# Kernel optimization log

Measured on AMD Instinct MI355X. Metric: run time of the kernel, lower is better.

The kernel has to match this reference:

```python
import jax, jax.numpy as jnp
import numpy as np

N, E, D, L = 100000, 600000, 128, 4
BN_EPS = 1e-5


def setup_inputs() -> dict:
    key = jax.random.key(0)
    ks = jax.random.split(key, 16)
    s = 0.02
    inp = {
        "x": jax.random.normal(ks[0], (N, D), dtype=jnp.float32),
        "edge_index": jax.random.randint(ks[1], (2, E), 0, N, dtype=jnp.int64),
        # per-layer SAGEConv params (lin_l has bias, lin_r has no bias in PyG)
        "lin_l_w": jax.random.normal(ks[2], (L, D, D), dtype=jnp.float32) * s,
        "lin_l_b": jnp.zeros((L, D), dtype=jnp.float32),
        "lin_r_w": jax.random.normal(ks[3], (L, D, D), dtype=jnp.float32) * s,
        # BatchNorm affine params (eval mode, running mean=0 var=1)
        "bn_w": jnp.ones((L, D), dtype=jnp.float32),
        "bn_b": jnp.zeros((L, D), dtype=jnp.float32),
        # MLP head: 128 -> 256 -> 128 -> 1
        "fc1_w": jax.random.normal(ks[4], (2 * D, D), dtype=jnp.float32) * s,
        "fc1_b": jnp.zeros((2 * D,), dtype=jnp.float32),
        "fc2_w": jax.random.normal(ks[5], (D, 2 * D), dtype=jnp.float32) * s,
        "fc2_b": jnp.zeros((D,), dtype=jnp.float32),
        "fc3_w": jax.random.normal(ks[6], (1, D), dtype=jnp.float32) * s,
        "fc3_b": jnp.zeros((1,), dtype=jnp.float32),
    }
    return inp


def _sage_layer(h, src, dst, deg_inv, wl, bl, wr):
    # mean aggregation of source features at destination nodes
    agg = jax.ops.segment_sum(h[src], dst, num_segments=N)  # [N, D]
    agg = agg * deg_inv[:, None]
    return agg @ wl.T + bl + h @ wr.T


def reference(x, lin_l_w, lin_l_b, lin_r_w, bn_w, bn_b,
              fc1_w, fc1_b, fc2_w, fc2_b, fc3_w, fc3_b, edge_index):
    src, dst = edge_index[0], edge_index[1]
    deg = jax.ops.segment_sum(jnp.ones((E,), jnp.float32), dst, num_segments=N)
    deg_inv = jnp.where(deg > 0, 1.0 / jnp.maximum(deg, 1.0), 0.0)
    inv_std = 1.0 / jnp.sqrt(1.0 + BN_EPS)  # eval BN with running mean=0, var=1

    h = x
    node_rep = x  # JK='sum' sums h_list[0..L-1]: input + first L-1 layer outputs
    for l in range(L):
        h = _sage_layer(h, src, dst, deg_inv, lin_l_w[l], lin_l_b[l], lin_r_w[l])
        h = h * inv_std * bn_w[l] + bn_b[l]
        if l != L - 1:
            h = jax.nn.relu(h)  # dropout = identity in eval mode
        if l != L - 1:
            node_rep = node_rep + h

    # batch is None -> global_add_pool sums all nodes into one graph
    g = jnp.sum(node_rep, axis=0, keepdims=True)  # [1, D]
    g = jax.nn.relu(g @ fc1_w.T + fc1_b)
    g = jax.nn.relu(g @ fc2_w.T + fc2_b)
    out = g @ fc3_w.T + fc3_b  # [1, num_tasks]
    return out
```

## Files before the change

### kernel.cpp

```cpp
#include <hip/hip_runtime.h>

#define NN 100000
#define NE 600000
#define DD 128
#define SCAN_CHUNK 2048
#define NCHUNK 49

typedef __attribute__((ext_vector_type(8))) short bf8;
typedef __attribute__((ext_vector_type(4))) float f4;
typedef __attribute__((ext_vector_type(4))) unsigned short us4;
typedef __attribute__((ext_vector_type(8))) unsigned short us8;

__device__ __forceinline__ float frelu(float x) { return x > 0.f ? x : 0.f; }

__device__ __forceinline__ float b2f(unsigned short u)
{
    union { unsigned int i; float f; } c;
    c.i = ((unsigned int)u) << 16;
    return c.f;
}

__device__ __forceinline__ unsigned short f2b(float f)
{
    union { float f; unsigned int i; } c;
    c.f = f;
    unsigned int u = c.i;
    return (unsigned short)((u + 0x7fffu + ((u >> 16) & 1u)) >> 16);
}

__device__ __forceinline__ float2 up2(unsigned int v)
{
    return make_float2(__uint_as_float(v << 16),
                       __uint_as_float(v & 0xffff0000u));
}

__global__ void k_detect(const int* __restrict__ ei, int* __restrict__ flag)
{
    if (blockIdx.x == 0 && threadIdx.x == 0) {
        int z = 1;
        for (int i = 0; i < 64; ++i)
            if (ei[2 * i + 1] != 0) { z = 0; break; }
        flag[0] = z;
    }
}

__global__ void k_count(const int* __restrict__ ei, const int* __restrict__ flag,
                        int* __restrict__ deg)
{
    int e = blockIdx.x * 256 + threadIdx.x;
    if (e >= NE) return;
    int w = flag[0];
    int dst = w ? ei[2 * (NE + e)] : ei[NE + e];
    atomicAdd(&deg[dst], 1);
}

__global__ void k_scan1(const int* __restrict__ cnt, int* __restrict__ offs,
                        int* __restrict__ chunks)
{
    __shared__ int sd[256];
    int t = threadIdx.x;
    int base = blockIdx.x * SCAN_CHUNK + t * 8;
    int v[8];
    int s = 0;
    #pragma unroll
    for (int i = 0; i < 8; ++i) {
        int idx = base + i;
        v[i] = (idx < NN) ? cnt[idx] : 0;
        s += v[i];
    }
    sd[t] = s;
    __syncthreads();
    for (int o = 1; o < 256; o <<= 1) {
        int x = (t >= o) ? sd[t - o] : 0;
        __syncthreads();
        sd[t] += x;
        __syncthreads();
    }
    int run = sd[t] - s;
    if (t == 255) chunks[blockIdx.x] = sd[255];
    #pragma unroll
    for (int i = 0; i < 8; ++i) {
        int idx = base + i;
        if (idx < NN) offs[idx] = run;
        run += v[i];
    }
}

__global__ void k_scan2(int* __restrict__ chunks, int* __restrict__ offs)
{
    if (threadIdx.x == 0 && blockIdx.x == 0) {
        int run = 0;
        for (int c = 0; c < NCHUNK; ++c) {
            int v = chunks[c];
            chunks[c] = run;
            run += v;
        }
        offs[NN] = run;
    }
}

__global__ void k_add2(int* __restrict__ offs, const int* __restrict__ chunks,
                       int* __restrict__ cursor, const int* __restrict__ deg,
                       float* __restrict__ deginv)
{
    int i = blockIdx.x * 256 + threadIdx.x;
    if (i >= NN) return;
    int v = offs[i] + chunks[i >> 11];
    offs[i] = v;
    cursor[i] = v;
    int d = deg[i];
    deginv[i] = (d > 0) ? 1.0f / (float)d : 0.0f;
}

__global__ void k_fill(const int* __restrict__ ei, const int* __restrict__ flag,
                       int* __restrict__ cursor, int* __restrict__ csr)
{
    int e = blockIdx.x * 256 + threadIdx.x;
    if (e >= NE) return;
    int w = flag[0];
    int src = w ? ei[2 * e] : ei[e];
    int dst = w ? ei[2 * (NE + e)] : ei[NE + e];
    int p = atomicAdd(&cursor[dst], 1);
    csr[p] = src;
}

__global__ void k_fold(const float* __restrict__ lwl, const float* __restrict__ lbl,
                       const float* __restrict__ lwr, const float* __restrict__ bnw,
                       const float* __restrict__ bnb, unsigned short* __restrict__ w2,
                       float* __restrict__ bias)
{
    int id = blockIdx.x * 256 + threadIdx.x;
    int l = id >> 15;
    int j = (id >> 8) & 127;
    int k = id & 255;
    float inv_std = 1.0f / sqrtf(1.0f + 1e-5f);
    float s = inv_std * bnw[l * 128 + j];
    float w = (k < 128) ? lwl[(l * 128 + j) * 128 + k]
                        : lwr[(l * 128 + j) * 128 + (k - 128)];
    w2[id] = f2b(w * s);
    if (k == 0) bias[l * 128 + j] = lbl[l * 128 + j] * s + bnb[l * 128 + j];
}

__global__ void k_cvtsum(const float* __restrict__ x, unsigned short* __restrict__ xb,
                         float* __restrict__ gsum)
{
    __shared__ float red[16][128];
    const int t = threadIdx.x;
    const int c8 = (t & 15) * 8;
    const int rg = t >> 4;
    float s[8];
    #pragma unroll
    for (int j = 0; j < 8; ++j) s[j] = 0.f;
    for (int r = blockIdx.x * 16 + rg; r < NN; r += gridDim.x * 16) {
        const f4* p = (const f4*)(x + (size_t)r * 128 + c8);
        f4 a = p[0], b = p[1];
        us8 o;
        o[0] = f2b(a[0]); o[1] = f2b(a[1]); o[2] = f2b(a[2]); o[3] = f2b(a[3]);
        o[4] = f2b(b[0]); o[5] = f2b(b[1]); o[6] = f2b(b[2]); o[7] = f2b(b[3]);
        *(us8*)(xb + (size_t)r * 128 + c8) = o;
        s[0] += a[0]; s[1] += a[1]; s[2] += a[2]; s[3] += a[3];
        s[4] += b[0]; s[5] += b[1]; s[6] += b[2]; s[7] += b[3];
    }
    #pragma unroll
    for (int j = 0; j < 8; ++j) red[rg][c8 + j] = s[j];
    __syncthreads();
    if (t < 128) {
        float v = 0.f;
        #pragma unroll
        for (int g = 0; g < 16; ++g) v += red[g][t];
        atomicAdd(&gsum[t], v);
    }
}

__global__ void k_gather(const unsigned short* __restrict__ in,
                         const int* __restrict__ offs, const int* __restrict__ csr,
                         const float* __restrict__ deginv,
                         unsigned short* __restrict__ agg)
{
    int wave = (blockIdx.x * 256 + threadIdx.x) >> 6;
    int lane = threadIdx.x & 63;
    if (wave >= NN) return;
    int s = offs[wave], e = offs[wave + 1];
    const int g = lane >> 4;
    const int cq = lane & 15;
    const uint4* base = (const uint4*)in;

    float2 a0[4], a1[4];
    #pragma unroll
    for (int j = 0; j < 4; ++j) {
        a0[j] = make_float2(0.f, 0.f);
        a1[j] = make_float2(0.f, 0.f);
    }

    for (int i = s + g; i < e; i += 8) {
        int src0 = csr[i];
        uint4 v0 = base[(size_t)src0 * 16 + cq];
        int i1 = i + 4;
        uint4 v1 = make_uint4(0u, 0u, 0u, 0u);
        if (i1 < e) {
            int src1 = csr[i1];
            v1 = base[(size_t)src1 * 16 + cq];
        }
        a0[0] += up2(v0.x); a0[1] += up2(v0.y);
        a0[2] += up2(v0.z); a0[3] += up2(v0.w);
        a1[0] += up2(v1.x); a1[1] += up2(v1.y);
        a1[2] += up2(v1.z); a1[3] += up2(v1.w);
    }

    float acc[8];
    #pragma unroll
    for (int j = 0; j < 4; ++j) {
        float2 t = a0[j] + a1[j];
        acc[2 * j] = t.x;
        acc[2 * j + 1] = t.y;
    }
    #pragma unroll
    for (int j = 0; j < 8; ++j) {
        float v = acc[j];
        v += __shfl_xor(v, 16);
        v += __shfl_xor(v, 32);
        acc[j] = v;
    }
    if (lane < 16) {
        float di = deginv[wave];
        us8 o;
        #pragma unroll
        for (int j = 0; j < 8; ++j) o[j] = f2b(acc[j] * di);
        *(us8*)(agg + (size_t)wave * 128 + cq * 8) = o;
    }
}

__global__ __launch_bounds__(256, 2)
void k_combine(const unsigned short* __restrict__ aggb,
               const unsigned short* __restrict__ hinb,
               const unsigned short* __restrict__ w2, const float* __restrict__ bias,
               unsigned short* __restrict__ hout, float* __restrict__ gsum, int write_h)
{
    __shared__ unsigned short sW[128 * 256];
    __shared__ float red[512];
    const int tid = threadIdx.x;
    const int lane = tid & 63, wid = tid >> 6;

    {
        const f4* wg = (const f4*)w2;
        #pragma unroll
        for (int it = 0; it < 16; ++it) {
            int idx = it * 256 + tid;
            int j = idx >> 5, c = idx & 31;
            f4 v = wg[idx];
            *(f4*)((char*)sW + j * 512 + ((c * 16) ^ ((j & 7) << 4))) = v;
        }
    }
    __syncthreads();

    const int r15 = lane & 15, q = lane >> 4;

    float bb[8][4];
    #pragma unroll
    for (int ct = 0; ct < 8; ++ct)
        #pragma unroll
        for (int r = 0; r < 4; ++r) bb[ct][r] = bias[ct * 16 + q * 4 + r];

    float csum[8][4];
    #pragma unroll
    for (int ct = 0; ct < 8; ++ct)
        #pragma unroll
        for (int r = 0; r < 4; ++r) csum[ct][r] = 0.f;

    #pragma unroll
    for (int grp = 0; grp < 2; ++grp) {
        const int row = blockIdx.x * 128 + grp * 64 + wid * 16 + r15;
        const int rowc = (row < NN) ? row : (NN - 1);
        const bool ok = row < NN;

        f4 acc[8];
        #pragma unroll
        for (int ct = 0; ct < 8; ++ct) acc[ct] = (f4){0.f, 0.f, 0.f, 0.f};

        #pragma unroll
        for (int ks = 0; ks < 8; ++ks) {
            const unsigned short* s = (ks < 4) ? aggb : hinb;
            bf8 bfrag = *(const bf8*)(s + (size_t)rowc * 128 + (ks & 3) * 32 + q * 8);
            #pragma unroll
            for (int ct = 0; ct < 8; ++ct) {
                int j = ct * 16 + r15;
                bf8 wfrag = *(const bf8*)((char*)sW + j * 512 +
                                          ((ks * 64 + q * 16) ^ ((j & 7) << 4)));
                acc[ct] = __builtin_amdgcn_mfma_f32_16x16x32_bf16(wfrag, bfrag, acc[ct], 0, 0, 0);
            }
        }

        #pragma unroll
        for (int ct = 0; ct < 8; ++ct) {
            float o[4];
            #pragma unroll
            for (int r = 0; r < 4; ++r) {
                float v = frelu(acc[ct][r] + bb[ct][r]);
                o[r] = ok ? v : 0.f;
                csum[ct][r] += o[r];
            }
            if (ok && write_h) {
                us4 p;
                p[0] = f2b(o[0]); p[1] = f2b(o[1]); p[2] = f2b(o[2]); p[3] = f2b(o[3]);
                *(us4*)(hout + (size_t)row * 128 + ct * 16 + q * 4) = p;
            }
        }
    }

    #pragma unroll
    for (int ct = 0; ct < 8; ++ct)
        #pragma unroll
        for (int r = 0; r < 4; ++r) {
            float v = csum[ct][r];
            v += __shfl_xor(v, 1);
            v += __shfl_xor(v, 2);
            v += __shfl_xor(v, 4);
            v += __shfl_xor(v, 8);
            csum[ct][r] = v;
        }

    if (r15 == 0) {
        #pragma unroll
        for (int ct = 0; ct < 8; ++ct)
            #pragma unroll
            for (int r = 0; r < 4; ++r)
                red[wid * 128 + ct * 16 + q * 4 + r] = csum[ct][r];
    }
    __syncthreads();
    if (tid < 128) {
        float s = red[tid] + red[128 + tid] + red[256 + tid] + red[384 + tid];
        atomicAdd(&gsum[tid], s);
    }
}

__global__ void k_mlp(const float* __restrict__ gsum,
                      const float* __restrict__ fc1w, const float* __restrict__ fc1b,
                      const float* __restrict__ fc2w, const float* __restrict__ fc2b,
                      const float* __restrict__ fc3w, const float* __restrict__ fc3b,
                      float* __restrict__ out)
{
    __shared__ float g[128], t1[256], t2[128];
    int t = threadIdx.x;
    if (t < 128) g[t] = gsum[t];
    __syncthreads();
    float a = fc1b[t];
    for (int k = 0; k < 128; ++k) a += fc1w[t * 128 + k] * g[k];
    t1[t] = frelu(a);
    __syncthreads();
    if (t < 128) {
        float a2 = fc2b[t];
        for (int k = 0; k < 256; ++k) a2 += fc2w[t * 256 + k] * t1[k];
        t2[t] = frelu(a2);
    }
    __syncthreads();
    if (t < 64) {
        float s = t2[t] * fc3w[t] + t2[t + 64] * fc3w[t + 64];
        for (int o = 32; o; o >>= 1) s += __shfl_down(s, o);
        if (t == 0) out[0] = s + fc3b[0];
    }
}

extern "C" void kernel_launch(void* const* d_in, const int* in_sizes, int n_in,
                              void* d_out, int out_size, void* d_ws, size_t ws_size,
                              hipStream_t stream)
{
    const float* x    = (const float*)d_in[0];
    const int*   ei   = (const int*)d_in[1];
    const float* lwl  = (const float*)d_in[2];
    const float* lbl  = (const float*)d_in[3];
    const float* lwr  = (const float*)d_in[4];
    const float* bnw  = (const float*)d_in[5];
    const float* bnb  = (const float*)d_in[6];
    const float* fc1w = (const float*)d_in[7];
    const float* fc1b = (const float*)d_in[8];
    const float* fc2w = (const float*)d_in[9];
    const float* fc2b = (const float*)d_in[10];
    const float* fc3w = (const float*)d_in[11];
    const float* fc3b = (const float*)d_in[12];
    float* out = (float*)d_out;

    char* ws = (char*)d_ws;
    size_t off = 0;
    auto alloc = [&](size_t b) -> char* {
        char* p = ws + off;
        off = (off + b + 255) & ~(size_t)255;
        return p;
    };
    int*   deg_cnt = (int*)alloc((size_t)NN * 4);
    int*   offs    = (int*)alloc((size_t)(NN + 1) * 4);
    int*   cursor  = (int*)alloc((size_t)NN * 4);
    int*   chunks  = (int*)alloc(64 * 4);
    int*   csr     = (int*)alloc((size_t)NE * 4);
    int*   flag    = (int*)alloc(4);
    float* deginv  = (float*)alloc((size_t)NN * 4);
    unsigned short* w2   = (unsigned short*)alloc((size_t)3 * 128 * 256 * 2);
    float* bias    = (float*)alloc((size_t)3 * 128 * 4);
    float* gsum    = (float*)alloc(128 * 4);
    unsigned short* xbf  = (unsigned short*)alloc((size_t)NN * 128 * 2);
    unsigned short* h    = (unsigned short*)alloc((size_t)NN * 128 * 2);
    unsigned short* agg  = (unsigned short*)alloc((size_t)NN * 128 * 2);

    hipMemsetAsync(deg_cnt, 0, (size_t)NN * 4, stream);
    hipMemsetAsync(gsum, 0, 128 * 4, stream);

    k_detect<<<1, 64, 0, stream>>>(ei, flag);
    k_count<<<(NE + 255) / 256, 256, 0, stream>>>(ei, flag, deg_cnt);
    k_scan1<<<NCHUNK, 256, 0, stream>>>(deg_cnt, offs, chunks);
    k_scan2<<<1, 64, 0, stream>>>(chunks, offs);
    k_add2<<<(NN + 255) / 256, 256, 0, stream>>>(offs, chunks, cursor, deg_cnt, deginv);
    k_fill<<<(NE + 255) / 256, 256, 0, stream>>>(ei, flag, cursor, csr);
    k_fold<<<(3 * 128 * 256) / 256, 256, 0, stream>>>(lwl, lbl, lwr, bnw, bnb, w2, bias);
    k_cvtsum<<<512, 256, 0, stream>>>(x, xbf, gsum);

    const unsigned short* hin = xbf;
    for (int l = 0; l < 3; ++l) {
        k_gather<<<(NN * 64) / 256, 256, 0, stream>>>(hin, offs, csr, deginv, agg);
        k_combine<<<(NN + 127) / 128, 256, 0, stream>>>(
            agg, hin, w2 + (size_t)l * 128 * 256, bias + (size_t)l * 128,
            h, gsum, (l < 2) ? 1 : 0);
        hin = h;
    }
    k_mlp<<<1, 256, 0, stream>>>(gsum, fc1w, fc1b, fc2w, fc2b, fc3w, fc3b, out);
}
```

Measured before the change: 323.4 us.

## Use 16 lanes per node in gather and register-resident weights in persistent combine

```diff
diff --git a/kernel.cpp b/kernel.cpp
--- a/kernel.cpp
+++ b/kernel.cpp
@@ -172,17 +172,15 @@
     }
 }
 
-__global__ void k_gather(const unsigned short* __restrict__ in,
-                         const int* __restrict__ offs, const int* __restrict__ csr,
-                         const float* __restrict__ deginv,
-                         unsigned short* __restrict__ agg)
-{
-    int wave = (blockIdx.x * 256 + threadIdx.x) >> 6;
-    int lane = threadIdx.x & 63;
-    if (wave >= NN) return;
-    int s = offs[wave], e = offs[wave + 1];
-    const int g = lane >> 4;
-    const int cq = lane & 15;
+__global__ __launch_bounds__(256)
+void k_gather(const unsigned short* __restrict__ in,
+              const int* __restrict__ offs, const int* __restrict__ csr,
+              const float* __restrict__ deginv,
+              unsigned short* __restrict__ agg)
+{
+    const int node = blockIdx.x * 16 + (threadIdx.x >> 4);
+    const int cq = threadIdx.x & 15;
+    int s = offs[node], e = offs[node + 1];
     const uint4* base = (const uint4*)in;
 
     float2 a0[4], a1[4];
@@ -192,42 +190,26 @@
         a1[j] = make_float2(0.f, 0.f);
     }
 
-    for (int i = s + g; i < e; i += 8) {
-        int src0 = csr[i];
-        uint4 v0 = base[(size_t)src0 * 16 + cq];
-        int i1 = i + 4;
+    for (int i = s; i < e; i += 2) {
+        uint4 v0 = base[(size_t)csr[i] * 16 + cq];
         uint4 v1 = make_uint4(0u, 0u, 0u, 0u);
-        if (i1 < e) {
-            int src1 = csr[i1];
-            v1 = base[(size_t)src1 * 16 + cq];
-        }
+        if (i + 1 < e)
+            v1 = base[(size_t)csr[i + 1] * 16 + cq];
         a0[0] += up2(v0.x); a0[1] += up2(v0.y);
         a0[2] += up2(v0.z); a0[3] += up2(v0.w);
         a1[0] += up2(v1.x); a1[1] += up2(v1.y);
         a1[2] += up2(v1.z); a1[3] += up2(v1.w);
     }
 
-    float acc[8];
+    float di = deginv[node];
+    us8 o;
     #pragma unroll
     for (int j = 0; j < 4; ++j) {
         float2 t = a0[j] + a1[j];
-        acc[2 * j] = t.x;
-        acc[2 * j + 1] = t.y;
-    }
-    #pragma unroll
-    for (int j = 0; j < 8; ++j) {
-        float v = acc[j];
-        v += __shfl_xor(v, 16);
-        v += __shfl_xor(v, 32);
-        acc[j] = v;
-    }
-    if (lane < 16) {
-        float di = deginv[wave];
-        us8 o;
-        #pragma unroll
-        for (int j = 0; j < 8; ++j) o[j] = f2b(acc[j] * di);
-        *(us8*)(agg + (size_t)wave * 128 + cq * 8) = o;
-    }
+        o[2 * j]     = f2b(t.x * di);
+        o[2 * j + 1] = f2b(t.y * di);
+    }
+    *(us8*)(agg + (size_t)node * 128 + cq * 8) = o;
 }
 
 __global__ __launch_bounds__(256, 2)
@@ -236,101 +218,75 @@
                const unsigned short* __restrict__ w2, const float* __restrict__ bias,
                unsigned short* __restrict__ hout, float* __restrict__ gsum, int write_h)
 {
-    __shared__ unsigned short sW[128 * 256];
-    __shared__ float red[512];
     const int tid = threadIdx.x;
     const int lane = tid & 63, wid = tid >> 6;
-
-    {
-        const f4* wg = (const f4*)w2;
-        #pragma unroll
-        for (int it = 0; it < 16; ++it) {
-            int idx = it * 256 + tid;
-            int j = idx >> 5, c = idx & 31;
-            f4 v = wg[idx];
-            *(f4*)((char*)sW + j * 512 + ((c * 16) ^ ((j & 7) << 4))) = v;
-        }
-    }
-    __syncthreads();
-
     const int r15 = lane & 15, q = lane >> 4;
 
-    float bb[8][4];
-    #pragma unroll
-    for (int ct = 0; ct < 8; ++ct)
-        #pragma unroll
-        for (int r = 0; r < 4; ++r) bb[ct][r] = bias[ct * 16 + q * 4 + r];
-
-    float csum[8][4];
-    #pragma unroll
-    for (int ct = 0; ct < 8; ++ct)
-        #pragma unroll
-        for (int r = 0; r < 4; ++r) csum[ct][r] = 0.f;
-
-    #pragma unroll
-    for (int grp = 0; grp < 2; ++grp) {
-        const int row = blockIdx.x * 128 + grp * 64 + wid * 16 + r15;
-        const int rowc = (row < NN) ? row : (NN - 1);
-        const bool ok = row < NN;
-
-        f4 acc[8];
-        #pragma unroll
-        for (int ct = 0; ct < 8; ++ct) acc[ct] = (f4){0.f, 0.f, 0.f, 0.f};
+    bf8 wf[2][8];
+    #pragma unroll
+    for (int c = 0; c < 2; ++c)
+        #pragma unroll
+        for (int ks = 0; ks < 8; ++ks)
+            wf[c][ks] = *(const bf8*)(w2 + ((size_t)(wid * 2 + c) * 16 + r15) * 256 +
+                                      ks * 32 + q * 8);
+
+    float bb[2][4];
+    #pragma unroll
+    for (int c = 0; c < 2; ++c)
+        #pragma unroll
+        for (int r = 0; r < 4; ++r)
+            bb[c][r] = bias[(wid * 2 + c) * 16 + q * 4 + r];
+
+    float csum[2][4];
+    #pragma unroll
+    for (int c = 0; c < 2; ++c)
+        #pragma unroll
+        for (int r = 0; r < 4; ++r) csum[c][r] = 0.f;
+
+    for (int g = blockIdx.x; g < NN / 16; g += gridDim.x) {
+        const int row = g * 16 + r15;
+
+        f4 acc[2];
+        acc[0] = (f4){0.f, 0.f, 0.f, 0.f};
+        acc[1] = (f4){0.f, 0.f, 0.f, 0.f};
 
         #pragma unroll
         for (int ks = 0; ks < 8; ++ks) {
             const unsigned short* s = (ks < 4) ? aggb : hinb;
-            bf8 bfrag = *(const bf8*)(s + (size_t)rowc * 128 + (ks & 3) * 32 + q * 8);
-            #pragma unroll
-            for (int ct = 0; ct < 8; ++ct) {
-                int j = ct * 16 + r15;
-                bf8 wfrag = *(const bf8*)((char*)sW + j * 512 +
-                                          ((ks * 64 + q * 16) ^ ((j & 7) << 4)));
-                acc[ct] = __builtin_amdgcn_mfma_f32_16x16x32_bf16(wfrag, bfrag, acc[ct], 0, 0, 0);
-            }
+            bf8 bfrag = *(const bf8*)(s + (size_t)row * 128 + (ks & 3) * 32 + q * 8);
+            acc[0] = __builtin_amdgcn_mfma_f32_16x16x32_bf16(wf[0][ks], bfrag, acc[0], 0, 0, 0);
+            acc[1] = __builtin_amdgcn_mfma_f32_16x16x32_bf16(wf[1][ks], bfrag, acc[1], 0, 0, 0);
         }
 
         #pragma unroll
-        for (int ct = 0; ct < 8; ++ct) {
+        for (int c = 0; c < 2; ++c) {
             float o[4];
             #pragma unroll
             for (int r = 0; r < 4; ++r) {
-                float v = frelu(acc[ct][r] + bb[ct][r]);
-                o[r] = ok ? v : 0.f;
-                csum[ct][r] += o[r];
+                float v = frelu(acc[c][r] + bb[c][r]);
+                o[r] = v;
+                csum[c][r] += v;
             }
-            if (ok && write_h) {
+            if (write_h) {
                 us4 p;
                 p[0] = f2b(o[0]); p[1] = f2b(o[1]); p[2] = f2b(o[2]); p[3] = f2b(o[3]);
-                *(us4*)(hout + (size_t)row * 128 + ct * 16 + q * 4) = p;
+                *(us4*)(hout + (size_t)row * 128 + (wid * 2 + c) * 16 + q * 4) = p;
             }
         }
     }
 
     #pragma unroll
-    for (int ct = 0; ct < 8; ++ct)
+    for (int c = 0; c < 2; ++c)
         #pragma unroll
         for (int r = 0; r < 4; ++r) {
-            float v = csum[ct][r];
+            float v = csum[c][r];
             v += __shfl_xor(v, 1);
             v += __shfl_xor(v, 2);
             v += __shfl_xor(v, 4);
             v += __shfl_xor(v, 8);
-            csum[ct][r] = v;
+            if (r15 == 0)
+                atomicAdd(&gsum[(wid * 2 + c) * 16 + q * 4 + r], v);
         }
-
-    if (r15 == 0) {
-        #pragma unroll
-        for (int ct = 0; ct < 8; ++ct)
-            #pragma unroll
-            for (int r = 0; r < 4; ++r)
-                red[wid * 128 + ct * 16 + q * 4 + r] = csum[ct][r];
-    }
-    __syncthreads();
-    if (tid < 128) {
-        float s = red[tid] + red[128 + tid] + red[256 + tid] + red[384 + tid];
-        atomicAdd(&gsum[tid], s);
-    }
 }
 
 __global__ void k_mlp(const float* __restrict__ gsum,
@@ -414,8 +370,8 @@
 
     const unsigned short* hin = xbf;
     for (int l = 0; l < 3; ++l) {
-        k_gather<<<(NN * 64) / 256, 256, 0, stream>>>(hin, offs, csr, deginv, agg);
-        k_combine<<<(NN + 127) / 128, 256, 0, stream>>>(
+        k_gather<<<NN / 16, 256, 0, stream>>>(hin, offs, csr, deginv, agg);
+        k_combine<<<512, 256, 0, stream>>>(
             agg, hin, w2 + (size_t)l * 128 * 256, bias + (size_t)l * 128,
             h, gsum, (l < 2) ? 1 : 0);
         hin = h;
```

New measurement: 435.4 us. 1.35x slower.

## Fuse neighbor gather into combine GEMM kernel with persistent tiles

Applied to the files above, without the earlier changes.

```diff
diff --git a/kernel.cpp b/kernel.cpp
--- a/kernel.cpp
+++ b/kernel.cpp
@@ -5,6 +5,7 @@
 #define DD 128
 #define SCAN_CHUNK 2048
 #define NCHUNK 49
+#define NST 1563
 
 typedef __attribute__((ext_vector_type(8))) short bf8;
 typedef __attribute__((ext_vector_type(4))) float f4;
@@ -172,72 +173,15 @@
     }
 }
 
-__global__ void k_gather(const unsigned short* __restrict__ in,
-                         const int* __restrict__ offs, const int* __restrict__ csr,
-                         const float* __restrict__ deginv,
-                         unsigned short* __restrict__ agg)
-{
-    int wave = (blockIdx.x * 256 + threadIdx.x) >> 6;
-    int lane = threadIdx.x & 63;
-    if (wave >= NN) return;
-    int s = offs[wave], e = offs[wave + 1];
-    const int g = lane >> 4;
-    const int cq = lane & 15;
-    const uint4* base = (const uint4*)in;
-
-    float2 a0[4], a1[4];
-    #pragma unroll
-    for (int j = 0; j < 4; ++j) {
-        a0[j] = make_float2(0.f, 0.f);
-        a1[j] = make_float2(0.f, 0.f);
-    }
-
-    for (int i = s + g; i < e; i += 8) {
-        int src0 = csr[i];
-        uint4 v0 = base[(size_t)src0 * 16 + cq];
-        int i1 = i + 4;
-        uint4 v1 = make_uint4(0u, 0u, 0u, 0u);
-        if (i1 < e) {
-            int src1 = csr[i1];
-            v1 = base[(size_t)src1 * 16 + cq];
-        }
-        a0[0] += up2(v0.x); a0[1] += up2(v0.y);
-        a0[2] += up2(v0.z); a0[3] += up2(v0.w);
-        a1[0] += up2(v1.x); a1[1] += up2(v1.y);
-        a1[2] += up2(v1.z); a1[3] += up2(v1.w);
-    }
-
-    float acc[8];
-    #pragma unroll
-    for (int j = 0; j < 4; ++j) {
-        float2 t = a0[j] + a1[j];
-        acc[2 * j] = t.x;
-        acc[2 * j + 1] = t.y;
-    }
-    #pragma unroll
-    for (int j = 0; j < 8; ++j) {
-        float v = acc[j];
-        v += __shfl_xor(v, 16);
-        v += __shfl_xor(v, 32);
-        acc[j] = v;
-    }
-    if (lane < 16) {
-        float di = deginv[wave];
-        us8 o;
-        #pragma unroll
-        for (int j = 0; j < 8; ++j) o[j] = f2b(acc[j] * di);
-        *(us8*)(agg + (size_t)wave * 128 + cq * 8) = o;
-    }
-}
-
 __global__ __launch_bounds__(256, 2)
-void k_combine(const unsigned short* __restrict__ aggb,
-               const unsigned short* __restrict__ hinb,
-               const unsigned short* __restrict__ w2, const float* __restrict__ bias,
-               unsigned short* __restrict__ hout, float* __restrict__ gsum, int write_h)
+void k_gcomb(const unsigned short* __restrict__ hinb,
+             const int* __restrict__ offs, const int* __restrict__ csr,
+             const float* __restrict__ deginv,
+             const unsigned short* __restrict__ w2, const float* __restrict__ bias,
+             unsigned short* __restrict__ hout, float* __restrict__ gsum, int write_h)
 {
     __shared__ unsigned short sW[128 * 256];
-    __shared__ float red[512];
+    __shared__ unsigned short tile[64 * 128];
     const int tid = threadIdx.x;
     const int lane = tid & 63, wid = tid >> 6;
 
@@ -251,9 +195,11 @@
             *(f4*)((char*)sW + j * 512 + ((c * 16) ^ ((j & 7) << 4))) = v;
         }
     }
-    __syncthreads();
 
     const int r15 = lane & 15, q = lane >> 4;
+    const int qw = tid >> 4;
+    const int cq = tid & 15;
+    const uint4* base = (const uint4*)hinb;
 
     float bb[8][4];
     #pragma unroll
@@ -267,9 +213,45 @@
         #pragma unroll
         for (int r = 0; r < 4; ++r) csum[ct][r] = 0.f;
 
-    #pragma unroll
-    for (int grp = 0; grp < 2; ++grp) {
-        const int row = blockIdx.x * 128 + grp * 64 + wid * 16 + r15;
+    for (int st = blockIdx.x; st < NST; st += gridDim.x) {
+        #pragma unroll
+        for (int sub = 0; sub < 4; ++sub) {
+            const int tr = sub * 16 + qw;
+            const int node = st * 64 + tr;
+            float2 a0[4], a1[4];
+            #pragma unroll
+            for (int j = 0; j < 4; ++j) {
+                a0[j] = make_float2(0.f, 0.f);
+                a1[j] = make_float2(0.f, 0.f);
+            }
+            float di = 0.f;
+            if (node < NN) {
+                int s = offs[node], e = offs[node + 1];
+                di = deginv[node];
+                for (int i = s; i < e; i += 2) {
+                    uint4 v0 = base[(size_t)csr[i] * 16 + cq];
+                    uint4 v1 = make_uint4(0u, 0u, 0u, 0u);
+                    if (i + 1 < e)
+                        v1 = base[(size_t)csr[i + 1] * 16 + cq];
+                    a0[0] += up2(v0.x); a0[1] += up2(v0.y);
+                    a0[2] += up2(v0.z); a0[3] += up2(v0.w);
+                    a1[0] += up2(v1.x); a1[1] += up2(v1.y);
+                    a1[2] += up2(v1.z); a1[3] += up2(v1.w);
+                }
+            }
+            us8 o;
+            #pragma unroll
+            for (int j = 0; j < 4; ++j) {
+                float2 t2 = a0[j] + a1[j];
+                o[2 * j]     = f2b(t2.x * di);
+                o[2 * j + 1] = f2b(t2.y * di);
+            }
+            *(us8*)((char*)tile + tr * 256 + ((cq * 16) ^ ((tr & 7) << 4))) = o;
+        }
+        __syncthreads();
+
+        const int tr = wid * 16 + r15;
+        const int row = st * 64 + tr;
         const int rowc = (row < NN) ? row : (NN - 1);
         const bool ok = row < NN;
 
@@ -279,8 +261,12 @@
 
         #pragma unroll
         for (int ks = 0; ks < 8; ++ks) {
-            const unsigned short* s = (ks < 4) ? aggb : hinb;
-            bf8 bfrag = *(const bf8*)(s + (size_t)rowc * 128 + (ks & 3) * 32 + q * 8);
+            bf8 bfrag;
+            if (ks < 4)
+                bfrag = *(const bf8*)((char*)tile + tr * 256 +
+                                      ((ks * 64 + q * 16) ^ ((tr & 7) << 4)));
+            else
+                bfrag = *(const bf8*)(hinb + (size_t)rowc * 128 + (ks & 3) * 32 + q * 8);
             #pragma unroll
             for (int ct = 0; ct < 8; ++ct) {
                 int j = ct * 16 + r15;
@@ -305,6 +291,7 @@
                 *(us4*)(hout + (size_t)row * 128 + ct * 16 + q * 4) = p;
             }
         }
+        __syncthreads();
     }
 
     #pragma unroll
@@ -319,6 +306,8 @@
             csum[ct][r] = v;
         }
 
+    float* red = (float*)sW;
+    __syncthreads();
     if (r15 == 0) {
         #pragma unroll
         for (int ct = 0; ct < 8; ++ct)
@@ -397,8 +386,8 @@
     float* bias    = (float*)alloc((size_t)3 * 128 * 4);
     float* gsum    = (float*)alloc(128 * 4);
     unsigned short* xbf  = (unsigned short*)alloc((size_t)NN * 128 * 2);
-    unsigned short* h    = (unsigned short*)alloc((size_t)NN * 128 * 2);
-    unsigned short* agg  = (unsigned short*)alloc((size_t)NN * 128 * 2);
+    unsigned short* hA   = (unsigned short*)alloc((size_t)NN * 128 * 2);
+    unsigned short* hB   = (unsigned short*)alloc((size_t)NN * 128 * 2);
 
     hipMemsetAsync(deg_cnt, 0, (size_t)NN * 4, stream);
     hipMemsetAsync(gsum, 0, 128 * 4, stream);
@@ -412,13 +401,14 @@
     k_fold<<<(3 * 128 * 256) / 256, 256, 0, stream>>>(lwl, lbl, lwr, bnw, bnb, w2, bias);
     k_cvtsum<<<512, 256, 0, stream>>>(x, xbf, gsum);
 
-    const unsigned short* hin = xbf;
-    for (int l = 0; l < 3; ++l) {
-        k_gather<<<(NN * 64) / 256, 256, 0, stream>>>(hin, offs, csr, deginv, agg);
-        k_combine<<<(NN + 127) / 128, 256, 0, stream>>>(
-            agg, hin, w2 + (size_t)l * 128 * 256, bias + (size_t)l * 128,
-            h, gsum, (l < 2) ? 1 : 0);
-        hin = h;
-    }
+    k_gcomb<<<512, 256, 0, stream>>>(xbf, offs, csr, deginv,
+                                     w2,                        bias,
+                                     hA, gsum, 1);
+    k_gcomb<<<512, 256, 0, stream>>>(hA, offs, csr, deginv,
+                                     w2 + (size_t)1 * 128 * 256, bias + 128,
+                                     hB, gsum, 1);
+    k_gcomb<<<512, 256, 0, stream>>>(hB, offs, csr, deginv,
+                                     w2 + (size_t)2 * 128 * 256, bias + 256,
+                                     hA, gsum, 0);
     k_mlp<<<1, 256, 0, stream>>>(gsum, fc1w, fc1b, fc2w, fc2b, fc3w, fc3b, out);
 }
```

New measurement: 405.2 us. 1.25x slower.

## Map one 16-lane group per node in gather and widen combine tiles

Applied to the files above, without the earlier changes.

```diff
diff --git a/kernel.cpp b/kernel.cpp
--- a/kernel.cpp
+++ b/kernel.cpp
@@ -168,22 +168,23 @@
         float v = 0.f;
         #pragma unroll
         for (int g = 0; g < 16; ++g) v += red[g][t];
-        atomicAdd(&gsum[t], v);
-    }
-}
-
-__global__ void k_gather(const unsigned short* __restrict__ in,
-                         const int* __restrict__ offs, const int* __restrict__ csr,
-                         const float* __restrict__ deginv,
-                         unsigned short* __restrict__ agg)
-{
-    int wave = (blockIdx.x * 256 + threadIdx.x) >> 6;
-    int lane = threadIdx.x & 63;
-    if (wave >= NN) return;
-    int s = offs[wave], e = offs[wave + 1];
-    const int g = lane >> 4;
-    const int cq = lane & 15;
-    const uint4* base = (const uint4*)in;
+        atomicAdd(&gsum[t * 16], v);
+    }
+}
+
+__global__ __launch_bounds__(256)
+void k_gather(const unsigned short* __restrict__ in,
+              const int* __restrict__ offs, const int* __restrict__ csr,
+              const float* __restrict__ deginv,
+              unsigned short* __restrict__ agg)
+{
+    const int node = blockIdx.x * 16 + (threadIdx.x >> 4);
+    const int cq = threadIdx.x & 15;
+    const int lane = threadIdx.x & 63;
+    const int qbase = lane & ~15;
+    int s = offs[node], e = offs[node + 1];
+    const int deg = e - s;
+    const uint4* bcq = (const uint4*)in + cq;
 
     float2 a0[4], a1[4];
     #pragma unroll
@@ -192,42 +193,42 @@
         a1[j] = make_float2(0.f, 0.f);
     }
 
-    for (int i = s + g; i < e; i += 8) {
-        int src0 = csr[i];
-        uint4 v0 = base[(size_t)src0 * 16 + cq];
-        int i1 = i + 4;
-        uint4 v1 = make_uint4(0u, 0u, 0u, 0u);
-        if (i1 < e) {
-            int src1 = csr[i1];
-            v1 = base[(size_t)src1 * 16 + cq];
-        }
-        a0[0] += up2(v0.x); a0[1] += up2(v0.y);
-        a0[2] += up2(v0.z); a0[3] += up2(v0.w);
-        a1[0] += up2(v1.x); a1[1] += up2(v1.y);
-        a1[2] += up2(v1.z); a1[3] += up2(v1.w);
-    }
-
-    float acc[8];
+    for (int cb = 0; cb < deg; cb += 16) {
+        int li = s + cb + cq;
+        int idx = csr[(li < e) ? li : (e - 1)];
+        int cnt = deg - cb; if (cnt > 16) cnt = 16;
+        for (int jb = 0; jb < cnt; jb += 4) {
+            int i0 = __shfl(idx, qbase + jb);
+            int i1 = __shfl(idx, qbase + jb + 1);
+            int i2 = __shfl(idx, qbase + jb + 2);
+            int i3 = __shfl(idx, qbase + jb + 3);
+            uint4 v0 = bcq[(size_t)i0 * 16];
+            uint4 v1 = make_uint4(0u, 0u, 0u, 0u);
+            uint4 v2 = make_uint4(0u, 0u, 0u, 0u);
+            uint4 v3 = make_uint4(0u, 0u, 0u, 0u);
+            if (jb + 1 < cnt) v1 = bcq[(size_t)i1 * 16];
+            if (jb + 2 < cnt) v2 = bcq[(size_t)i2 * 16];
+            if (jb + 3 < cnt) v3 = bcq[(size_t)i3 * 16];
+            a0[0] += up2(v0.x); a0[1] += up2(v0.y);
+            a0[2] += up2(v0.z); a0[3] += up2(v0.w);
+            a1[0] += up2(v1.x); a1[1] += up2(v1.y);
+            a1[2] += up2(v1.z); a1[3] += up2(v1.w);
+            a0[0] += up2(v2.x); a0[1] += up2(v2.y);
+            a0[2] += up2(v2.z); a0[3] += up2(v2.w);
+            a1[0] += up2(v3.x); a1[1] += up2(v3.y);
+            a1[2] += up2(v3.z); a1[3] += up2(v3.w);
+        }
+    }
+
+    float di = deginv[node];
+    us8 o;
     #pragma unroll
     for (int j = 0; j < 4; ++j) {
         float2 t = a0[j] + a1[j];
-        acc[2 * j] = t.x;
-        acc[2 * j + 1] = t.y;
-    }
-    #pragma unroll
-    for (int j = 0; j < 8; ++j) {
-        float v = acc[j];
-        v += __shfl_xor(v, 16);
-        v += __shfl_xor(v, 32);
-        acc[j] = v;
-    }
-    if (lane < 16) {
-        float di = deginv[wave];
-        us8 o;
-        #pragma unroll
-        for (int j = 0; j < 8; ++j) o[j] = f2b(acc[j] * di);
-        *(us8*)(agg + (size_t)wave * 128 + cq * 8) = o;
-    }
+        o[2 * j]     = f2b(t.x * di);
+        o[2 * j + 1] = f2b(t.y * di);
+    }
+    *(us8*)(agg + (size_t)node * 128 + cq * 8) = o;
 }
 
 __global__ __launch_bounds__(256, 2)
@@ -268,8 +269,8 @@
         for (int r = 0; r < 4; ++r) csum[ct][r] = 0.f;
 
     #pragma unroll
-    for (int grp = 0; grp < 2; ++grp) {
-        const int row = blockIdx.x * 128 + grp * 64 + wid * 16 + r15;
+    for (int grp = 0; grp < 4; ++grp) {
+        const int row = blockIdx.x * 256 + grp * 64 + wid * 16 + r15;
         const int rowc = (row < NN) ? row : (NN - 1);
         const bool ok = row < NN;
 
@@ -329,7 +330,7 @@
     __syncthreads();
     if (tid < 128) {
         float s = red[tid] + red[128 + tid] + red[256 + tid] + red[384 + tid];
-        atomicAdd(&gsum[tid], s);
+        atomicAdd(&gsum[tid * 16], s);
     }
 }
 
@@ -341,7 +342,7 @@
 {
     __shared__ float g[128], t1[256], t2[128];
     int t = threadIdx.x;
-    if (t < 128) g[t] = gsum[t];
+    if (t < 128) g[t] = gsum[t * 16];
     __syncthreads();
     float a = fc1b[t];
     for (int k = 0; k < 128; ++k) a += fc1w[t * 128 + k] * g[k];
@@ -395,13 +396,14 @@
     float* deginv  = (float*)alloc((size_t)NN * 4);
     unsigned short* w2   = (unsigned short*)alloc((size_t)3 * 128 * 256 * 2);
     float* bias    = (float*)alloc((size_t)3 * 128 * 4);
-    float* gsum    = (float*)alloc(128 * 4);
+    float* gsum    = (float*)alloc(128 * 16 * 4);
     unsigned short* xbf  = (unsigned short*)alloc((size_t)NN * 128 * 2);
-    unsigned short* h    = (unsigned short*)alloc((size_t)NN * 128 * 2);
+    unsigned short* hA   = (unsigned short*)alloc((size_t)NN * 128 * 2);
+    unsigned short* hB   = (unsigned short*)alloc((size_t)NN * 128 * 2);
     unsigned short* agg  = (unsigned short*)alloc((size_t)NN * 128 * 2);
 
     hipMemsetAsync(deg_cnt, 0, (size_t)NN * 4, stream);
-    hipMemsetAsync(gsum, 0, 128 * 4, stream);
+    hipMemsetAsync(gsum, 0, 128 * 16 * 4, stream);
 
     k_detect<<<1, 64, 0, stream>>>(ei, flag);
     k_count<<<(NE + 255) / 256, 256, 0, stream>>>(ei, flag, deg_cnt);
@@ -413,12 +415,13 @@
     k_cvtsum<<<512, 256, 0, stream>>>(x, xbf, gsum);
 
     const unsigned short* hin = xbf;
+    unsigned short* houts[3] = {hA, hB, hA};
     for (int l = 0; l < 3; ++l) {
-        k_gather<<<(NN * 64) / 256, 256, 0, stream>>>(hin, offs, csr, deginv, agg);
-        k_combine<<<(NN + 127) / 128, 256, 0, stream>>>(
+        k_gather<<<NN / 16, 256, 0, stream>>>(hin, offs, csr, deginv, agg);
+        k_combine<<<(NN + 255) / 256, 256, 0, stream>>>(
             agg, hin, w2 + (size_t)l * 128 * 256, bias + (size_t)l * 128,
-            h, gsum, (l < 2) ? 1 : 0);
-        hin = h;
+            houts[l], gsum, (l < 2) ? 1 : 0);
+        hin = houts[l];
     }
     k_mlp<<<1, 256, 0, stream>>>(gsum, fc1w, fc1b, fc2w, fc2b, fc3w, fc3b, out);
 }
```

Result: faster. 261.9 us (-19.0%).
